# Optimization experiments

Hardware: AMD Instinct MI355X
Metric: run time of the kernel (lower is better)

## Reference

```python
import jax, jax.numpy as jnp
import numpy as np

N_NODES = 100000
N_EDGES = 1600000
IN_SIZE = 512
HID_SIZE = 256
OUT_SIZE = 40
K_STEPS = 10
ALPHA = 0.1


def setup_inputs() -> dict:
    key = jax.random.key(0)
    ks = jax.random.split(key, 8)
    features = jax.random.normal(ks[0], (N_NODES, IN_SIZE), dtype=jnp.float32)
    src = jax.random.randint(ks[1], (N_EDGES,), 0, N_NODES, dtype=jnp.int64)
    dst = jax.random.randint(ks[2], (N_EDGES,), 0, N_NODES, dtype=jnp.int64)
    # MLP params (Kaiming-ish scale)
    W1 = jax.random.normal(ks[3], (IN_SIZE, HID_SIZE), dtype=jnp.float32) / np.sqrt(IN_SIZE)
    b1 = jnp.zeros((HID_SIZE,), dtype=jnp.float32)
    W2 = jax.random.normal(ks[4], (HID_SIZE, OUT_SIZE), dtype=jnp.float32) / np.sqrt(HID_SIZE)
    b2 = jnp.zeros((OUT_SIZE,), dtype=jnp.float32)
    return {"features": features, "src": src, "dst": dst,
            "W1": W1, "b1": b1, "W2": W2, "b2": b2}


def reference(features, src, dst, W1, b1, W2, b2):
    # --- MLP encoder (dropout is identity in eval mode) ---
    h = jax.nn.relu(features @ W1 + b1)
    h = h @ W2 + b2  # [N, out_size]

    # --- Symmetric normalization (DGL APPNPConv, edge_weight=None) ---
    ones_e = jnp.ones((src.shape[0],), dtype=h.dtype)
    deg_out = jax.ops.segment_sum(ones_e, src, num_segments=N_NODES)
    deg_in = jax.ops.segment_sum(ones_e, dst, num_segments=N_NODES)
    norm_src = jnp.power(jnp.clip(deg_out, 1.0), -0.5)[:, None]  # D_out^{-1/2}
    norm_dst = jnp.power(jnp.clip(deg_in, 1.0), -0.5)[:, None]   # D_in^{-1/2}

    # --- k=10 APPNP propagation: h <- (1-a) * D^{-1/2} A D^{-1/2} h + a * h0 ---
    h0 = h

    def step(h, _):
        msg = (h * norm_src)[src]                                  # gather [E, out]
        agg = jax.ops.segment_sum(msg, dst, num_segments=N_NODES)  # scatter-add
        h = (1.0 - ALPHA) * (agg * norm_dst) + ALPHA * h0
        return h, None

    h, _ = jax.lax.scan(step, h, None, length=K_STEPS)
    return h
```

## Files before the change

### kernel.cpp

```cpp
#include <hip/hip_runtime.h>

#define N_NODES 100000
#define N_EDGES 1600000
#define IN_SIZE 512
#define HID_SIZE 256
#define OUT_SIZE 40
#define K_STEPS 10
#define ALPHA 0.1f

#define NCH 250
#define CH_E 6400
#define NBUK 391
#define NRS 8
#define HRS 12544
#define NCS 16
#define CS_E 100000

typedef _Float16 half8 __attribute__((ext_vector_type(8)));
typedef float f32x4 __attribute__((ext_vector_type(4)));

struct __align__(8) Entry { int s; int d; };

__device__ inline void gld_lds16(const void* g, void* l) {
    __builtin_amdgcn_global_load_lds(
        (const __attribute__((address_space(1))) void*)g,
        (__attribute__((address_space(3))) void*)l,
        16, 0, 0);
}

__global__ __launch_bounds__(512) void hist_pass(const int* __restrict__ dst,
                                                 int* __restrict__ cnt) {
    __shared__ int h[NBUK];
    const int t = threadIdx.x, c = blockIdx.x;
    for (int j = t; j < NBUK; j += 512) h[j] = 0;
    __syncthreads();
    const int4* d4 = (const int4*)(dst + c * CH_E);
    for (int i = t; i < CH_E / 4; i += 512) {
        const int4 v = d4[i];
        atomicAdd(&h[v.x >> 8], 1);
        atomicAdd(&h[v.y >> 8], 1);
        atomicAdd(&h[v.z >> 8], 1);
        atomicAdd(&h[v.w >> 8], 1);
    }
    __syncthreads();
    for (int j = t; j < NBUK; j += 512) cnt[c * NBUK + j] = h[j];
}

__global__ __launch_bounds__(512) void bucket_scan(const int* __restrict__ cnt,
                                                   int* __restrict__ off,
                                                   int* __restrict__ boff) {
    __shared__ int tot[512];
    const int b = threadIdx.x;
    int s = 0;
    if (b < NBUK)
        for (int c = 0; c < NCH; ++c) s += cnt[c * NBUK + b];
    tot[b] = s;
    __syncthreads();
    for (int o = 1; o < 512; o <<= 1) {
        const int v = (b >= o) ? tot[b - o] : 0;
        __syncthreads();
        tot[b] += v;
        __syncthreads();
    }
    if (b < NBUK) {
        int run = tot[b] - s;
        boff[b] = run;
        for (int c = 0; c < NCH; ++c) { off[c * NBUK + b] = run; run += cnt[c * NBUK + b]; }
        if (b == NBUK - 1) boff[NBUK] = tot[b];
    }
}

__global__ __launch_bounds__(512) void scatter_pass(const int* __restrict__ src,
                                                    const int* __restrict__ dst,
                                                    const int* __restrict__ off,
                                                    Entry* __restrict__ ebuf) {
    __shared__ int cur[NBUK];
    const int t = threadIdx.x, c = blockIdx.x;
    for (int j = t; j < NBUK; j += 512) cur[j] = off[c * NBUK + j];
    __syncthreads();
    const int4* s4 = (const int4*)(src + c * CH_E);
    const int4* d4 = (const int4*)(dst + c * CH_E);
    for (int i = t; i < CH_E / 4; i += 512) {
        const int4 sv = s4[i];
        const int4 dv = d4[i];
        Entry e;
        int p;
        p = atomicAdd(&cur[dv.x >> 8], 1); e.s = sv.x; e.d = dv.x; ebuf[p] = e;
        p = atomicAdd(&cur[dv.y >> 8], 1); e.s = sv.y; e.d = dv.y; ebuf[p] = e;
        p = atomicAdd(&cur[dv.z >> 8], 1); e.s = sv.z; e.d = dv.z; ebuf[p] = e;
        p = atomicAdd(&cur[dv.w >> 8], 1); e.s = sv.w; e.d = dv.w; ebuf[p] = e;
    }
}

__global__ __launch_bounds__(256) void bucket_csr(const Entry* __restrict__ ebuf,
                                                  const int* __restrict__ boff,
                                                  int* __restrict__ rowp,
                                                  float* __restrict__ ndst,
                                                  int* __restrict__ csr) {
    __shared__ int hist[256];
    __shared__ int pref[256];
    __shared__ int cur[256];
    const int t = threadIdx.x, b = blockIdx.x;
    const int beg = boff[b], end = boff[b + 1];
    hist[t] = 0;
    __syncthreads();
    for (int i = beg + t; i < end; i += 256)
        atomicAdd(&hist[ebuf[i].d & 255], 1);
    __syncthreads();
    const int h = hist[t];
    pref[t] = h;
    __syncthreads();
    for (int o = 1; o < 256; o <<= 1) {
        const int v = (t >= o) ? pref[t - o] : 0;
        __syncthreads();
        pref[t] += v;
        __syncthreads();
    }
    const int val = beg + pref[t] - h;
    const int n = (b << 8) + t;
    if (n <= N_NODES) rowp[n] = val;
    if (n < N_NODES) ndst[n] = 1.0f / sqrtf((float)max(h, 1));
    cur[t] = val;
    __syncthreads();
    for (int i = beg + t; i < end; i += 256) {
        const Entry e = ebuf[i];
        const int pos = atomicAdd(&cur[e.d & 255], 1);
        csr[pos] = e.s;
    }
}

__global__ __launch_bounds__(512) void degsrc_part(const int* __restrict__ src,
                                                   int* __restrict__ partial) {
    __shared__ int h[HRS];
    const int t = threadIdx.x;
    const int r = blockIdx.x & (NRS - 1);
    const int c = blockIdx.x >> 3;
    const int base = r * HRS;
    for (int j = t; j < HRS; j += 512) h[j] = 0;
    __syncthreads();
    const int4* s4 = (const int4*)(src + (size_t)c * CS_E);
    for (int i = t; i < CS_E / 4; i += 512) {
        const int4 v = s4[i];
        unsigned u;
        u = (unsigned)(v.x - base); if (u < HRS) atomicAdd(&h[u], 1);
        u = (unsigned)(v.y - base); if (u < HRS) atomicAdd(&h[u], 1);
        u = (unsigned)(v.z - base); if (u < HRS) atomicAdd(&h[u], 1);
        u = (unsigned)(v.w - base); if (u < HRS) atomicAdd(&h[u], 1);
    }
    __syncthreads();
    for (int j = t; j < HRS; j += 512) partial[(size_t)c * (NRS * HRS) + base + j] = h[j];
}

__global__ __launch_bounds__(256) void nsrc_reduce(const int* __restrict__ partial,
                                                   float* __restrict__ nsrc) {
    const int n = blockIdx.x * 256 + threadIdx.x;
    int s = 0;
#pragma unroll
    for (int c = 0; c < NCS; ++c) s += partial[(size_t)c * (NRS * HRS) + n];
    if (n < N_NODES) nsrc[n] = 1.0f / sqrtf((float)max(s, 1));
}

__global__ __launch_bounds__(256) void prep_w1tp(const float* __restrict__ W1,
                                                 unsigned short* __restrict__ w1tp) {
    int idx = blockIdx.x * 256 + threadIdx.x;
    if (idx < IN_SIZE * HID_SIZE) {
        const int kt  = idx >> 14;
        const int p   = idx & 16383;
        const int n   = p >> 6;
        const int off = p & 63;
        const int j   = off & 7;
        const int ch  = (off >> 3) ^ (n & 7);
        const int kg  = kt * 64 + ch * 8 + j;
        _Float16 h = (_Float16)W1[(size_t)kg * HID_SIZE + n];
        w1tp[idx] = *(unsigned short*)&h;
    }
}

__global__ __launch_bounds__(512) void gemm1_f16(const float* __restrict__ X,
                                                 const unsigned short* __restrict__ w1tp,
                                                 const float* __restrict__ b1,
                                                 _Float16* __restrict__ h1) {
    __shared__ __align__(16) _Float16 sA[128 * 64];
    __shared__ __align__(16) _Float16 sB[256 * 64];

    const int t    = threadIdx.x;
    const int lane = t & 63;
    const int w    = t >> 6;
    const int wr   = w >> 2;
    const int wc   = w & 3;
    const int n0   = blockIdx.x * 128;

    f32x4 acc[4][4];
#pragma unroll
    for (int i = 0; i < 4; ++i)
#pragma unroll
        for (int j = 0; j < 4; ++j) acc[i][j] = (f32x4)0.f;

    const int lo = lane & 15;
    const int hi = lane >> 4;
    const int l7 = lane & 7;

    for (int kk = 0; kk < IN_SIZE; kk += 64) {
        __syncthreads();
        {
            const unsigned short* gsrc = w1tp + ((size_t)(kk >> 6) << 14);
#pragma unroll
            for (int i = 0; i < 4; ++i) {
                const int c = t + i * 512;
                gld_lds16(gsrc + c * 8, &sB[c * 8]);
            }
        }
#pragma unroll
        for (int i = 0; i < 2; ++i) {
            int id  = t + i * 512;
            int row = id >> 3;
            int ch  = id & 7;
            int gr  = n0 + row;
            float4 x0 = make_float4(0.f, 0.f, 0.f, 0.f), x1 = x0;
            if (gr < N_NODES) {
                const float* p = X + (size_t)gr * IN_SIZE + kk + ch * 8;
                x0 = ((const float4*)p)[0];
                x1 = ((const float4*)p)[1];
            }
            half8 hv;
            hv[0] = (_Float16)x0.x; hv[1] = (_Float16)x0.y;
            hv[2] = (_Float16)x0.z; hv[3] = (_Float16)x0.w;
            hv[4] = (_Float16)x1.x; hv[5] = (_Float16)x1.y;
            hv[6] = (_Float16)x1.z; hv[7] = (_Float16)x1.w;
            *(half8*)&sA[row * 64 + ((ch ^ (row & 7)) << 3)] = hv;
        }
        __syncthreads();
#pragma unroll
        for (int s = 0; s < 2; ++s) {
            const int chs = ((s * 4 + hi) ^ l7) << 3;
            half8 af[4], bf[4];
#pragma unroll
            for (int f = 0; f < 4; ++f)
                af[f] = *(const half8*)&sA[(wr * 64 + f * 16 + lo) * 64 + chs];
#pragma unroll
            for (int f = 0; f < 4; ++f)
                bf[f] = *(const half8*)&sB[(wc * 64 + f * 16 + lo) * 64 + chs];
#pragma unroll
            for (int fi = 0; fi < 4; ++fi)
#pragma unroll
                for (int fj = 0; fj < 4; ++fj)
                    acc[fi][fj] = __builtin_amdgcn_mfma_f32_16x16x32_f16(
                        af[fi], bf[fj], acc[fi][fj], 0, 0, 0);
        }
    }

    float b1v[4];
#pragma unroll
    for (int fj = 0; fj < 4; ++fj) b1v[fj] = b1[wc * 64 + fj * 16 + lo];
#pragma unroll
    for (int fi = 0; fi < 4; ++fi) {
#pragma unroll
        for (int fj = 0; fj < 4; ++fj) {
            const int col = wc * 64 + fj * 16 + lo;
#pragma unroll
            for (int r = 0; r < 4; ++r) {
                int grow = n0 + wr * 64 + fi * 16 + hi * 4 + r;
                if (grow < N_NODES) {
                    float v = acc[fi][fj][r] + b1v[fj];
                    v = fmaxf(v, 0.f);
                    h1[(size_t)grow * HID_SIZE + col] = (_Float16)v;
                }
            }
        }
    }
}

__global__ __launch_bounds__(256) void gemm2(const _Float16* __restrict__ h1,
                                             const float* __restrict__ W2,
                                             const float* __restrict__ b2,
                                             float* __restrict__ h0) {
    __shared__ __align__(16) float sW2t[40 * 260];
    __shared__ __align__(16) unsigned short sH[64 * 264];

    const int t  = threadIdx.x;
    const int n0 = blockIdx.x * 64;

    for (int idx = t; idx < HID_SIZE * OUT_SIZE; idx += 256) {
        int c = idx / OUT_SIZE;
        int o = idx - c * OUT_SIZE;
        sW2t[o * 260 + c] = W2[idx];
    }
#pragma unroll
    for (int i = 0; i < 8; ++i) {
        int id  = t + i * 256;
        int row = id >> 5;
        int ch  = id & 31;
        uint4 v = make_uint4(0, 0, 0, 0);
        if (n0 + row < N_NODES)
            v = *(const uint4*)(h1 + (size_t)(n0 + row) * HID_SIZE + ch * 8);
        *(uint4*)&sH[row * 264 + ch * 8] = v;
    }
    __syncthreads();

    const int r2 = t >> 2;
    const int q  = t & 3;
    const int o0 = q * 10;
    float acc2[10];
#pragma unroll
    for (int m = 0; m < 10; ++m) acc2[m] = b2[o0 + m];

    for (int c = 0; c < HID_SIZE; c += 8) {
        uint4 hv = *(const uint4*)&sH[r2 * 264 + c];
        const _Float16* hp = (const _Float16*)&hv;
        float f[8];
#pragma unroll
        for (int j = 0; j < 8; ++j) f[j] = (float)hp[j];
#pragma unroll
        for (int m = 0; m < 10; ++m) {
            const float4 w0 = *(const float4*)&sW2t[(o0 + m) * 260 + c];
            const float4 w1 = *(const float4*)&sW2t[(o0 + m) * 260 + c + 4];
            acc2[m] += f[0] * w0.x + f[1] * w0.y + f[2] * w0.z + f[3] * w0.w
                     + f[4] * w1.x + f[5] * w1.y + f[6] * w1.z + f[7] * w1.w;
        }
    }
    if (n0 + r2 < N_NODES) {
        float* dstp = h0 + (size_t)(n0 + r2) * OUT_SIZE + o0;
#pragma unroll
        for (int m = 0; m < 10; ++m) dstp[m] = acc2[m];
    }
}

__global__ __launch_bounds__(320) void g0_init(const float* __restrict__ h0,
                                               const float* __restrict__ nsrc,
                                               _Float16* __restrict__ g) {
    const int tid = threadIdx.x;
    const int ln  = tid / 5;
    const int q   = tid - ln * 5;
    const int n   = blockIdx.x * 64 + ln;
    if (n >= N_NODES) return;
    const float ns = nsrc[n];
    const f32x4 a = *(const f32x4*)(h0 + (size_t)n * OUT_SIZE + q * 8);
    const f32x4 b = *(const f32x4*)(h0 + (size_t)n * OUT_SIZE + q * 8 + 4);
    half8 gv;
    gv[0] = (_Float16)(ns * a[0]); gv[1] = (_Float16)(ns * a[1]);
    gv[2] = (_Float16)(ns * a[2]); gv[3] = (_Float16)(ns * a[3]);
    gv[4] = (_Float16)(ns * b[0]); gv[5] = (_Float16)(ns * b[1]);
    gv[6] = (_Float16)(ns * b[2]); gv[7] = (_Float16)(ns * b[3]);
    *(half8*)(g + (size_t)n * 64 + q * 8) = gv;
}

__global__ __launch_bounds__(320) void appnp_step3(const _Float16* __restrict__ gin,
                                                   const float* __restrict__ h0,
                                                   const int* __restrict__ rowp,
                                                   const int* __restrict__ csr,
                                                   const float* __restrict__ nsrc,
                                                   const float* __restrict__ ndst,
                                                   _Float16* __restrict__ gout,
                                                   float* __restrict__ hout,
                                                   int last) {
    const int tid = threadIdx.x;
    const int ln  = tid / 5;
    const int q   = tid - ln * 5;
    const int n   = blockIdx.x * 64 + ln;
    if (n >= N_NODES) return;

    const int beg = rowp[n];
    const int end = rowp[n + 1];
    const _Float16* gq = gin + q * 8;

    float acc[8];
#pragma unroll
    for (int j = 0; j < 8; ++j) acc[j] = 0.f;

    int e = beg;
    for (; e + 4 <= end; e += 4) {
        const int s0 = csr[e + 0];
        const int s1 = csr[e + 1];
        const int s2 = csr[e + 2];
        const int s3 = csr[e + 3];
        const half8 v0 = *(const half8*)(gq + (size_t)s0 * 64);
        const half8 v1 = *(const half8*)(gq + (size_t)s1 * 64);
        const half8 v2 = *(const half8*)(gq + (size_t)s2 * 64);
        const half8 v3 = *(const half8*)(gq + (size_t)s3 * 64);
#pragma unroll
        for (int j = 0; j < 8; ++j)
            acc[j] += (float)v0[j] + (float)v1[j] + (float)v2[j] + (float)v3[j];
    }
    for (; e < end; ++e) {
        const int s0 = csr[e];
        const half8 v0 = *(const half8*)(gq + (size_t)s0 * 64);
#pragma unroll
        for (int j = 0; j < 8; ++j) acc[j] += (float)v0[j];
    }

    const float nd = (1.0f - ALPHA) * ndst[n];
    const f32x4 h0a = *(const f32x4*)(h0 + (size_t)n * OUT_SIZE + q * 8);
    const f32x4 h0b = *(const f32x4*)(h0 + (size_t)n * OUT_SIZE + q * 8 + 4);
    float r[8];
    r[0] = nd * acc[0] + ALPHA * h0a[0]; r[1] = nd * acc[1] + ALPHA * h0a[1];
    r[2] = nd * acc[2] + ALPHA * h0a[2]; r[3] = nd * acc[3] + ALPHA * h0a[3];
    r[4] = nd * acc[4] + ALPHA * h0b[0]; r[5] = nd * acc[5] + ALPHA * h0b[1];
    r[6] = nd * acc[6] + ALPHA * h0b[2]; r[7] = nd * acc[7] + ALPHA * h0b[3];

    if (last) {
        f32x4 ra, rb;
        ra[0] = r[0]; ra[1] = r[1]; ra[2] = r[2]; ra[3] = r[3];
        rb[0] = r[4]; rb[1] = r[5]; rb[2] = r[6]; rb[3] = r[7];
        *(f32x4*)(hout + (size_t)n * OUT_SIZE + q * 8) = ra;
        *(f32x4*)(hout + (size_t)n * OUT_SIZE + q * 8 + 4) = rb;
    } else {
        const float ns = nsrc[n];
        half8 gv;
#pragma unroll
        for (int j = 0; j < 8; ++j) gv[j] = (_Float16)(ns * r[j]);
        *(half8*)(gout + (size_t)n * 64 + q * 8) = gv;
    }
}

extern "C" void kernel_launch(void* const* d_in, const int* in_sizes, int n_in,
                              void* d_out, int out_size, void* d_ws, size_t ws_size,
                              hipStream_t stream) {
    const float* X   = (const float*)d_in[0];
    const int*   src = (const int*)d_in[1];
    const int*   dst = (const int*)d_in[2];
    const float* W1  = (const float*)d_in[3];
    const float* b1  = (const float*)d_in[4];
    const float* W2  = (const float*)d_in[5];
    const float* b2  = (const float*)d_in[6];
    float* out = (float*)d_out;

    char* ws = (char*)d_ws;
    size_t off = 0;
    auto alloc = [&](size_t bytes) -> void* {
        void* p = ws + off;
        off = (off + bytes + 255) & ~(size_t)255;
        return p;
    };
    float* h0 = (float*)alloc((size_t)N_NODES * OUT_SIZE * 4);
    const size_t mark = off;

    unsigned short* w1tp = (unsigned short*)alloc((size_t)IN_SIZE * HID_SIZE * 2);
    _Float16*       h1   = (_Float16*)alloc((size_t)N_NODES * HID_SIZE * 2);

    off = mark;
    _Float16* gA = (_Float16*)alloc((size_t)N_NODES * 64 * 2);
    _Float16* gB = (_Float16*)alloc((size_t)N_NODES * 64 * 2);
    int*   partial = (int*)gA;
    Entry* ebuf    = (Entry*)gB;
    float* nsrc = (float*)alloc((size_t)N_NODES * 4);
    float* ndst = (float*)alloc((size_t)N_NODES * 4);
    int* rowp   = (int*)alloc((size_t)(N_NODES + 2) * 4);
    int* csr    = (int*)alloc((size_t)N_EDGES * 4);
    int* cnt    = (int*)alloc((size_t)NCH * NBUK * 4);
    int* offb   = (int*)alloc((size_t)NCH * NBUK * 4);
    int* boff   = (int*)alloc((size_t)(NBUK + 1) * 4);

    const int pgrid = (N_NODES + 63) / 64;

    prep_w1tp<<<(IN_SIZE * HID_SIZE + 255) / 256, 256, 0, stream>>>(W1, w1tp);
    gemm1_f16<<<(N_NODES + 127) / 128, 512, 0, stream>>>(X, w1tp, b1, h1);
    gemm2<<<(N_NODES + 63) / 64, 256, 0, stream>>>(h1, W2, b2, h0);

    hist_pass<<<NCH, 512, 0, stream>>>(dst, cnt);
    bucket_scan<<<1, 512, 0, stream>>>(cnt, offb, boff);
    scatter_pass<<<NCH, 512, 0, stream>>>(src, dst, offb, ebuf);
    bucket_csr<<<NBUK, 256, 0, stream>>>(ebuf, boff, rowp, ndst, csr);

    degsrc_part<<<NRS * NCS, 512, 0, stream>>>(src, partial);
    nsrc_reduce<<<(NRS * HRS) / 256, 256, 0, stream>>>(partial, nsrc);

    g0_init<<<pgrid, 320, 0, stream>>>(h0, nsrc, gA);

    const _Float16* gin = gA;
    for (int s = 0; s < K_STEPS; ++s) {
        const int last = (s == K_STEPS - 1) ? 1 : 0;
        _Float16* gout = (s & 1) ? gA : gB;
        appnp_step3<<<pgrid, 320, 0, stream>>>(gin, h0, rowp, csr, nsrc, ndst,
                                               gout, out, last);
        gin = gout;
    }
}
```

Before: 550.3 us.

## Store hidden activations transposed and rewrite second GEMM as per-node column kernel

The first GEMM epilogue now writes ReLU outputs into a transposed, node-padded layout using 4-wide half stores instead of per-element row-major stores. The second GEMM is replaced by a kernel where each thread owns one node, streams its 256 hidden values with coalesced loads across threads, and accumulates 40 outputs against W2 broadcast from shared memory. This aims to cut LDS staging and the reduction overhead of the old gemm2. The cost is strided, less coalesced writes in gemm1 and high register pressure from 40 accumulators.

```diff
diff --git a/kernel.cpp b/kernel.cpp
--- a/kernel.cpp
+++ b/kernel.cpp
@@ -7,6 +7,7 @@
 #define OUT_SIZE 40
 #define K_STEPS 10
 #define ALPHA 0.1f
+#define NP 100096
 
 #define NCH 250
 #define CH_E 6400
@@ -17,6 +18,7 @@
 #define CS_E 100000
 
 typedef _Float16 half8 __attribute__((ext_vector_type(8)));
+typedef _Float16 half4 __attribute__((ext_vector_type(4)));
 typedef float f32x4 __attribute__((ext_vector_type(4)));
 
 struct __align__(8) Entry { int s; int d; };
@@ -179,7 +181,7 @@
 __global__ __launch_bounds__(512) void gemm1_f16(const float* __restrict__ X,
                                                  const unsigned short* __restrict__ w1tp,
                                                  const float* __restrict__ b1,
-                                                 _Float16* __restrict__ h1) {
+                                                 _Float16* __restrict__ h1t) {
     __shared__ __align__(16) _Float16 sA[128 * 64];
     __shared__ __align__(16) _Float16 sB[256 * 64];
 
@@ -254,74 +256,48 @@
     for (int fj = 0; fj < 4; ++fj) b1v[fj] = b1[wc * 64 + fj * 16 + lo];
 #pragma unroll
     for (int fi = 0; fi < 4; ++fi) {
+        const int nb = n0 + wr * 64 + fi * 16 + hi * 4;
 #pragma unroll
         for (int fj = 0; fj < 4; ++fj) {
-            const int col = wc * 64 + fj * 16 + lo;
-#pragma unroll
-            for (int r = 0; r < 4; ++r) {
-                int grow = n0 + wr * 64 + fi * 16 + hi * 4 + r;
-                if (grow < N_NODES) {
-                    float v = acc[fi][fj][r] + b1v[fj];
-                    v = fmaxf(v, 0.f);
-                    h1[(size_t)grow * HID_SIZE + col] = (_Float16)v;
-                }
-            }
+            const int c = wc * 64 + fj * 16 + lo;
+            half4 hv;
+#pragma unroll
+            for (int r = 0; r < 4; ++r)
+                hv[r] = (_Float16)fmaxf(acc[fi][fj][r] + b1v[fj], 0.f);
+            *(half4*)(h1t + (size_t)c * NP + nb) = hv;
         }
     }
 }
 
-__global__ __launch_bounds__(256) void gemm2(const _Float16* __restrict__ h1,
-                                             const float* __restrict__ W2,
-                                             const float* __restrict__ b2,
-                                             float* __restrict__ h0) {
-    __shared__ __align__(16) float sW2t[40 * 260];
-    __shared__ __align__(16) unsigned short sH[64 * 264];
-
-    const int t  = threadIdx.x;
-    const int n0 = blockIdx.x * 64;
-
-    for (int idx = t; idx < HID_SIZE * OUT_SIZE; idx += 256) {
-        int c = idx / OUT_SIZE;
-        int o = idx - c * OUT_SIZE;
-        sW2t[o * 260 + c] = W2[idx];
-    }
-#pragma unroll
-    for (int i = 0; i < 8; ++i) {
-        int id  = t + i * 256;
-        int row = id >> 5;
-        int ch  = id & 31;
-        uint4 v = make_uint4(0, 0, 0, 0);
-        if (n0 + row < N_NODES)
-            v = *(const uint4*)(h1 + (size_t)(n0 + row) * HID_SIZE + ch * 8);
-        *(uint4*)&sH[row * 264 + ch * 8] = v;
-    }
-    __syncthreads();
-
-    const int r2 = t >> 2;
-    const int q  = t & 3;
-    const int o0 = q * 10;
-    float acc2[10];
-#pragma unroll
-    for (int m = 0; m < 10; ++m) acc2[m] = b2[o0 + m];
-
-    for (int c = 0; c < HID_SIZE; c += 8) {
-        uint4 hv = *(const uint4*)&sH[r2 * 264 + c];
-        const _Float16* hp = (const _Float16*)&hv;
-        float f[8];
-#pragma unroll
-        for (int j = 0; j < 8; ++j) f[j] = (float)hp[j];
-#pragma unroll
-        for (int m = 0; m < 10; ++m) {
-            const float4 w0 = *(const float4*)&sW2t[(o0 + m) * 260 + c];
-            const float4 w1 = *(const float4*)&sW2t[(o0 + m) * 260 + c + 4];
-            acc2[m] += f[0] * w0.x + f[1] * w0.y + f[2] * w0.z + f[3] * w0.w
-                     + f[4] * w1.x + f[5] * w1.y + f[6] * w1.z + f[7] * w1.w;
-        }
-    }
-    if (n0 + r2 < N_NODES) {
-        float* dstp = h0 + (size_t)(n0 + r2) * OUT_SIZE + o0;
-#pragma unroll
-        for (int m = 0; m < 10; ++m) dstp[m] = acc2[m];
+__global__ __launch_bounds__(256) void gemm2t(const _Float16* __restrict__ h1t,
+                                              const float* __restrict__ W2,
+                                              const float* __restrict__ b2,
+                                              float* __restrict__ h0) {
+    __shared__ float sW2[HID_SIZE * OUT_SIZE];
+    const int t = threadIdx.x;
+    const int n = blockIdx.x * 256 + t;
+    for (int i = t; i < HID_SIZE * OUT_SIZE; i += 256) sW2[i] = W2[i];
+    __syncthreads();
+
+    float acc[OUT_SIZE];
+#pragma unroll
+    for (int o = 0; o < OUT_SIZE; ++o) acc[o] = b2[o];
+
+    const _Float16* hp = h1t + n;
+#pragma unroll 4
+    for (int c = 0; c < HID_SIZE; ++c) {
+        const float hv = (float)hp[(size_t)c * NP];
+        const float* wrow = &sW2[c * OUT_SIZE];
+#pragma unroll
+        for (int o = 0; o < OUT_SIZE; ++o)
+            acc[o] = fmaf(hv, wrow[o], acc[o]);
+    }
+
+    if (n < N_NODES) {
+        float* dst = h0 + (size_t)n * OUT_SIZE;
+#pragma unroll
+        for (int o = 0; o < OUT_SIZE; o += 4)
+            *(f32x4*)(dst + o) = *(f32x4*)&acc[o];
     }
 }
 
@@ -435,7 +411,7 @@
     const size_t mark = off;
 
     unsigned short* w1tp = (unsigned short*)alloc((size_t)IN_SIZE * HID_SIZE * 2);
-    _Float16*       h1   = (_Float16*)alloc((size_t)N_NODES * HID_SIZE * 2);
+    _Float16*       h1t  = (_Float16*)alloc((size_t)HID_SIZE * NP * 2);
 
     off = mark;
     _Float16* gA = (_Float16*)alloc((size_t)N_NODES * 64 * 2);
@@ -451,10 +427,11 @@
     int* boff   = (int*)alloc((size_t)(NBUK + 1) * 4);
 
     const int pgrid = (N_NODES + 63) / 64;
+    const int ngrid256 = (N_NODES + 255) / 256;
 
     prep_w1tp<<<(IN_SIZE * HID_SIZE + 255) / 256, 256, 0, stream>>>(W1, w1tp);
-    gemm1_f16<<<(N_NODES + 127) / 128, 512, 0, stream>>>(X, w1tp, b1, h1);
-    gemm2<<<(N_NODES + 63) / 64, 256, 0, stream>>>(h1, W2, b2, h0);
+    gemm1_f16<<<(N_NODES + 127) / 128, 512, 0, stream>>>(X, w1tp, b1, h1t);
+    gemm2t<<<ngrid256, 256, 0, stream>>>(h1t, W2, b2, h0);
 
     hist_pass<<<NCH, 512, 0, stream>>>(dst, cnt);
     bucket_scan<<<1, 512, 0, stream>>>(cnt, offb, boff);
```

After: 556.3 us. About the same (+1.1%).
